# Performance work log

Measured on AMD Instinct MI355X. Metric: run time of the kernel, lower is better.

The kernel has to match this reference:

```python
import jax, jax.numpy as jnp
import numpy as np

N = 100000          # nodes
E = 1600000         # edges
KS = 3              # kernel_size per dim
DIM = 3             # pseudo-coordinate dim
CH = [1, 8, 16, 32, 16, 8, 1]
_BITS = ((0,0,0),(1,0,0),(0,1,0),(1,1,0),(0,0,1),(1,0,1),(0,1,1),(1,1,1))
_STRIDES = (1, KS, KS * KS)


def setup_inputs() -> dict:
    key = jax.random.key(0)
    ks = jax.random.split(key, 32)
    inp = {
        "x": jax.random.normal(ks[0], (N, 1), jnp.float32),
        "edge_index": jax.random.randint(ks[1], (2, E), 0, N),
        "pseudo": jax.random.uniform(ks[2], (E, DIM), dtype=jnp.float32),
    }
    ki = 3
    for i in range(6):
        fi, fo = CH[i], CH[i + 1]
        inp[f"w{i+1}"] = jax.random.normal(ks[ki], (KS**DIM, fi, fo), jnp.float32) / np.float32(np.sqrt(fi * 8)); ki += 1
        inp[f"root{i+1}"] = jax.random.normal(ks[ki], (fi, fo), jnp.float32) / np.float32(np.sqrt(fi)); ki += 1
        inp[f"b{i+1}"] = jnp.zeros((fo,), jnp.float32); ki += 1
    return inp


def spline_conv(x, src, dst, pseudo, W, root, bias):
    """Degree-1 open B-spline SplineConv, sum aggregation (norm=False) + root + bias.
    x: [N,Fin], pseudo: [E,DIM] in [0,1], W: [27,Fin,Fout]."""
    v = pseudo * (KS - 1)                              # [E,DIM] in [0,KS-1]
    f = jnp.clip(jnp.floor(v), 0.0, KS - 2)           # left knot per dim
    frac = v - f                                       # fractional part
    fi = f.astype(jnp.int32)
    # transform every node by all 27 kernel matrices once: [N,27,Fout]
    xw = jnp.einsum('nf,kfo->nko', x, W)
    m = jnp.zeros((src.shape[0], W.shape[-1]), x.dtype)
    for bits in _BITS:                                 # 2^DIM = 8 nonzero basis fns
        w = jnp.ones((src.shape[0],), x.dtype)
        idx = jnp.zeros((src.shape[0],), jnp.int32)
        for d in range(DIM):
            w = w * (frac[:, d] if bits[d] else (1.0 - frac[:, d]))
            idx = idx + (fi[:, d] + bits[d]) * _STRIDES[d]
        m = m + w[:, None] * xw[src, idx]              # gather [E,Fout]
    out = jax.ops.segment_sum(m, dst, num_segments=x.shape[0])
    return out + x @ root + bias


def reference(x, edge_index, pseudo, w1, root1, b1, w2, root2, b2, w3, root3, b3,
              w4, root4, b4, w5, root5, b5, w6, root6, b6):
    src, dst = edge_index[0], edge_index[1]
    h = x
    for (W, R, B) in ((w1, root1, b1), (w2, root2, b2), (w3, root3, b3),
                      (w4, root4, b4), (w5, root5, b5), (w6, root6, b6)):
        h = jax.nn.elu(spline_conv(h, src, dst, pseudo, W, R, B))
    return h.reshape(-1)
```

## Files before the change

kernel.cpp:

```cpp
#include <hip/hip_runtime.h>
#include <hip/hip_fp16.h>

#define N_NODES 100000
#define N_EDGES 1600000
#define TS      1024
#define NTILE   ((N_NODES + TS - 1) / TS)
#define NGRP    (NTILE * 8)
#define E_PAD2  (N_EDGES + NGRP * 64 + 256)
#define GRID_E2 (E_PAD2 / 256)

typedef _Float16 f16x8 __attribute__((ext_vector_type(8)));
typedef float    f32x4 __attribute__((ext_vector_type(4)));


__device__ __forceinline__ void pseudo_to_of(float p0, float p1, float p2,
                                             int& oct, float& fr0, float& fr1, float& fr2) {
    float v0 = p0 * 2.0f, v1 = p1 * 2.0f, v2 = p2 * 2.0f;
    int i0 = v0 >= 1.0f, i1 = v1 >= 1.0f, i2 = v2 >= 1.0f;
    fr0 = v0 - (float)i0; fr1 = v1 - (float)i1; fr2 = v2 - (float)i2;
    oct = i0 + 2 * i1 + 4 * i2;
}

template<int Fin>
__device__ __forceinline__ void loadanyT(const float* __restrict__ hp, float* x) {
    if constexpr (Fin % 4 == 0) {
        const float4* xv = reinterpret_cast<const float4*>(hp);
        #pragma unroll
        for (int f = 0; f < Fin / 4; ++f) {
            float4 t = xv[f];
            x[4*f+0] = t.x; x[4*f+1] = t.y; x[4*f+2] = t.z; x[4*f+3] = t.w;
        }
    } else {
        #pragma unroll
        for (int f = 0; f < Fin; ++f) x[f] = hp[f];
    }
}

template<int Fin>
__device__ __forceinline__ void loadanyT(const __half* __restrict__ hp, float* x) {
    if constexpr (Fin % 8 == 0) {
        #pragma unroll
        for (int r = 0; r < Fin / 8; ++r) {
            union { uint4 v; __half2 h2[4]; } u;
            u.v = ((const uint4*)hp)[r];
            #pragma unroll
            for (int q = 0; q < 4; ++q) {
                float2 f = __half22float2(u.h2[q]);
                x[r*8 + 2*q]     = f.x;
                x[r*8 + 2*q + 1] = f.y;
            }
        }
    } else {
        #pragma unroll
        for (int f = 0; f < Fin; ++f) x[f] = __half2float(hp[f]);
    }
}

template<int CH>
__device__ __forceinline__ void storeanyT(float* __restrict__ p, const float* z) {
    if constexpr (CH % 4 == 0) {
        #pragma unroll
        for (int o = 0; o < CH / 4; ++o) {
            float4 t; t.x = z[4*o]; t.y = z[4*o+1]; t.z = z[4*o+2]; t.w = z[4*o+3];
            ((float4*)p)[o] = t;
        }
    } else if constexpr (CH % 2 == 0) {
        #pragma unroll
        for (int o = 0; o < CH / 2; ++o) {
            float2 t; t.x = z[2*o]; t.y = z[2*o+1];
            ((float2*)p)[o] = t;
        }
    } else {
        #pragma unroll
        for (int o = 0; o < CH; ++o) p[o] = z[o];
    }
}

template<int CH>
__device__ __forceinline__ void storeanyT(__half* __restrict__ p, const float* z) {
    if constexpr (CH % 8 == 0) {
        #pragma unroll
        for (int q = 0; q < CH / 8; ++q) {
            union { uint4 v; __half2 h2[4]; } u;
            #pragma unroll
            for (int r = 0; r < 4; ++r)
                u.h2[r] = __floats2half2_rn(z[q*8 + 2*r], z[q*8 + 2*r + 1]);
            ((uint4*)p)[q] = u.v;
        }
    } else if constexpr (CH % 4 == 0) {
        #pragma unroll
        for (int q = 0; q < CH / 4; ++q) {
            union { uint2 v; __half2 h2[2]; } u;
            u.h2[0] = __floats2half2_rn(z[4*q],     z[4*q + 1]);
            u.h2[1] = __floats2half2_rn(z[4*q + 2], z[4*q + 3]);
            ((uint2*)p)[q] = u.v;
        }
    } else if constexpr (CH % 2 == 0) {
        #pragma unroll
        for (int q = 0; q < CH / 2; ++q)
            ((__half2*)p)[q] = __floats2half2_rn(z[2*q], z[2*q+1]);
    } else {
        #pragma unroll
        for (int o = 0; o < CH; ++o) p[o] = __float2half(z[o]);
    }
}

template<int CH>
__device__ __forceinline__ void accum_m_f16(float* acc, const __half* __restrict__ p) {
    if constexpr (CH % 8 == 0) {
        #pragma unroll
        for (int q = 0; q < CH / 8; ++q) {
            union { uint4 v; __half2 h2[4]; } u;
            u.v = ((const uint4*)p)[q];
            #pragma unroll
            for (int r = 0; r < 4; ++r) {
                float2 f = __half22float2(u.h2[r]);
                acc[q*8 + 2*r]     += f.x;
                acc[q*8 + 2*r + 1] += f.y;
            }
        }
    } else if constexpr (CH % 2 == 0) {
        #pragma unroll
        for (int q = 0; q < CH / 2; ++q) {
            float2 f = __half22float2(((const __half2*)p)[q]);
            acc[2*q] += f.x; acc[2*q+1] += f.y;
        }
    } else {
        #pragma unroll
        for (int o = 0; o < CH; ++o) acc[o] += __half2float(p[o]);
    }
}

__device__ __forceinline__ int cnt_unpack(unsigned v, int half) {
    return (int)((v >> (half * 16)) & 0xFFFFu);
}


__global__ __launch_bounds__(256) void count8_k(const int* __restrict__ dst,
                                                const float* __restrict__ pseudo,
                                                unsigned* __restrict__ cnt4,
                                                unsigned short* __restrict__ rank16) {
    int e = blockIdx.x * 256 + threadIdx.x;
    if (e >= N_EDGES) return;
    int d = dst[e];
    size_t pb = (size_t)e * 3;
    int oct; float a, b, c;
    pseudo_to_of(pseudo[pb], pseudo[pb + 1], pseudo[pb + 2], oct, a, b, c);
    unsigned inc = 1u << ((oct & 1) * 16);
    unsigned r = atomicAdd(&cnt4[d * 4 + (oct >> 1)], inc);
    rank16[e] = (unsigned short)cnt_unpack(r, oct & 1);
}

__global__ __launch_bounds__(256) void scan_g1(const unsigned* __restrict__ cnt4,
                                               int* __restrict__ gsum) {
    __shared__ int red[256];
    int g = blockIdx.x, t = threadIdx.x;
    int tile = g >> 3, oct = g & 7;
    int s = 0;
    #pragma unroll
    for (int q = 0; q < 4; ++q) {
        int n = tile * TS + t * 4 + q;
        if (n < N_NODES) s += cnt_unpack(cnt4[n * 4 + (oct >> 1)], oct & 1);
    }
    red[t] = s;
    __syncthreads();
    #pragma unroll
    for (int off = 128; off > 0; off >>= 1) {
        if (t < off) red[t] += red[t + off];
        __syncthreads();
    }
    if (t == 0) gsum[g] = red[0];
}

__global__ __launch_bounds__(1024) void scan_g2(const int* __restrict__ gsum,
                                                int* __restrict__ gbase,
                                                int* __restrict__ tot,
                                                unsigned char* __restrict__ winoct,
                                                uint4* __restrict__ slotmeta) {
    __shared__ int s[1024];
    __shared__ int sraw;
    int t = threadIdx.x;
    int v = 0;
    if (t < NGRP) v = ((gsum[t] + 63) >> 6) << 6;
    s[t] = v;
    __syncthreads();
    #pragma unroll
    for (int off = 1; off < 1024; off <<= 1) {
        int u = (t >= off) ? s[t - off] : 0;
        __syncthreads();
        s[t] += u;
        __syncthreads();
    }
    if (t < NGRP) gbase[t] = s[t] - v;
    if (t == NGRP - 1) sraw = s[t];
    __syncthreads();
    int raw = sraw;
    int totp = (raw + 255) & ~255;
    if (t == 0) { tot[0] = raw; tot[1] = totp; }
    int fill = totp - raw;
    if (t < fill) {
        uint4 z; z.x = z.y = z.z = z.w = 0u;
        slotmeta[raw + t] = z;
    }
    if (t < (fill >> 6)) winoct[(raw >> 6) + t] = 0;
}

__global__ __launch_bounds__(256) void scan_g3(const unsigned* __restrict__ cnt4,
                                               const int* __restrict__ gbase,
                                               int* __restrict__ slotstart,
                                               unsigned char* __restrict__ winoct,
                                               uint4* __restrict__ slotmeta) {
    __shared__ int s[256];
    int g = blockIdx.x, t = threadIdx.x;
    int tile = g >> 3, oct = g & 7;
    int c[4];
    int sum = 0;
    #pragma unroll
    for (int q = 0; q < 4; ++q) {
        int n = tile * TS + t * 4 + q;
        c[q] = (n < N_NODES) ? cnt_unpack(cnt4[n * 4 + (oct >> 1)], oct & 1) : 0;
        sum += c[q];
    }
    s[t] = sum;
    __syncthreads();
    #pragma unroll
    for (int off = 1; off < 256; off <<= 1) {
        int u = (t >= off) ? s[t - off] : 0;
        __syncthreads();
        s[t] += u;
        __syncthreads();
    }
    int base = gbase[g];
    int run = base + s[t] - sum;
    #pragma unroll
    for (int q = 0; q < 4; ++q) {
        int n = tile * TS + t * 4 + q;
        if (n < N_NODES) { slotstart[n * 8 + oct] = run; run += c[q]; }
    }
    int cntg = s[255];
    int padded = ((cntg + 63) >> 6) << 6;
    for (int w = t; w < (padded >> 6); w += 256)
        winoct[(base >> 6) + w] = (unsigned char)oct;
    for (int i = t; i < padded - cntg; i += 256) {
        uint4 z; z.x = z.y = z.z = z.w = 0u;
        slotmeta[base + cntg + i] = z;
    }
}

__global__ __launch_bounds__(256) void scatter2_k(const int* __restrict__ src,
                                                  const int* __restrict__ dst,
                                                  const float* __restrict__ pseudo,
                                                  const unsigned short* __restrict__ rank16,
                                                  const int* __restrict__ slotstart,
                                                  uint4* __restrict__ slotmeta) {
    int e = blockIdx.x * 256 + threadIdx.x;
    if (e >= N_EDGES) return;
    int d = dst[e];
    size_t pb = (size_t)e * 3;
    int oct; float fr0, fr1, fr2;
    pseudo_to_of(pseudo[pb], pseudo[pb + 1], pseudo[pb + 2], oct, fr0, fr1, fr2);
    int slot = slotstart[d * 8 + oct] + (int)rank16[e];
    union { uint4 v; struct { int s; __half2 f01; __half2 f2x; unsigned pad; } t; } su;
    su.t.s   = src[e];
    su.t.f01 = __floats2half2_rn(fr0, fr1);
    su.t.f2x = __floats2half2_rn(fr2, 0.0f);
    su.t.pad = 0u;
    slotmeta[slot] = su.v;
}


template<int Fin, int Fout>
__device__ __forceinline__ void wprep_elem(const float* __restrict__ W,
                                           _Float16* __restrict__ WB, int i) {
    constexpr int KT = (8 * Fin) / 32;
    constexpr int NT = (Fout + 15) / 16;
    int j    = i & 7;
    int lane = (i >> 3) & 63;
    int rest = i >> 9;
    int nt = rest % NT; rest /= NT;
    int kt = rest % KT;
    int g  = rest / KT;
    int kb = lane >> 4, n = lane & 15;
    int k  = kt * 32 + kb * 8 + j;
    int b  = k / Fin, f = k % Fin;
    int bidx = (g & 1) + 3 * ((g >> 1) & 1) + 9 * ((g >> 2) & 1);
    int idx  = bidx + (b & 1) + 3 * ((b >> 1) & 1) + 9 * ((b >> 2) & 1);
    int col  = nt * 16 + n;
    float v = (col < Fout) ? W[((size_t)idx * Fin + f) * Fout + col] : 0.0f;
    WB[i] = (_Float16)v;
}

#define WS2 8192
#define WS3 32768
#define WS4 32768
#define WS5 16384

__global__ __launch_bounds__(256) void wprep_all_k(const float* __restrict__ W2,
                                                   const float* __restrict__ W3,
                                                   const float* __restrict__ W4,
                                                   const float* __restrict__ W5,
                                                   _Float16* __restrict__ WB2,
                                                   _Float16* __restrict__ WB3,
                                                   _Float16* __restrict__ WB4,
                                                   _Float16* __restrict__ WB5) {
    int i = blockIdx.x * 256 + threadIdx.x;
    if (i < WS2) { wprep_elem<8, 16>(W2, WB2, i); return; }
    i -= WS2;
    if (i < WS3) { wprep_elem<16, 32>(W3, WB3, i); return; }
    i -= WS3;
    if (i < WS4) { wprep_elem<32, 16>(W4, WB4, i); return; }
    i -= WS4;
    if (i < WS5) { wprep_elem<16, 8>(W5, WB5, i); return; }
}


template<int Fin, int Fout>
__global__ __launch_bounds__(256) void msg_mfma_k(const __half* __restrict__ h,
                                                  const uint4* __restrict__ slotmeta,
                                                  const unsigned char* __restrict__ winoct,
                                                  const int* __restrict__ tot,
                                                  const _Float16* __restrict__ WB,
                                                  __half* __restrict__ m) {
    constexpr int KT = (8 * Fin) / 32;
    constexpr int NT = (Fout + 15) / 16;
    constexpr int LOG2FIN = (Fin == 8) ? 3 : (Fin == 16) ? 4 : 5;
    constexpr int ZR = NT * 16 + 8;

    __shared__ __align__(16) _Float16 zbuf[4][64 * ZR];

    const int base = blockIdx.x * 256;
    if (base >= tot[1]) return;

    const int tid = threadIdx.x, wv = tid >> 6, lane = tid & 63;
    const int slot = base + tid;
    const int wbase = base + wv * 64;
    const int kb = lane >> 4;

    int oct = winoct[(base >> 6) + wv];
    oct = __builtin_amdgcn_readfirstlane(oct);

    int   sE[4];
    float g0[4], h0[4], g1[4], h1[4], g2[4], h2v[4];
    #pragma unroll
    for (int mt = 0; mt < 4; ++mt) {
        union { uint4 v; struct { int s; __half2 f01; __half2 f2x; unsigned pad; } t; } u;
        u.v = slotmeta[wbase + mt * 16 + (lane & 15)];
        sE[mt] = u.t.s;
        float2 f01 = __half22float2(u.t.f01);
        float2 f2x = __half22float2(u.t.f2x);
        g0[mt] = 1.0f - f01.x; h0[mt] = f01.x;
        g1[mt] = 1.0f - f01.y; h1[mt] = f01.y;
        g2[mt] = 1.0f - f2x.x; h2v[mt] = f2x.x;
    }

    f32x4 acc[4][NT];
    #pragma unroll
    for (int mt = 0; mt < 4; ++mt)
        #pragma unroll
        for (int nt = 0; nt < NT; ++nt)
            acc[mt][nt] = (f32x4){0.0f, 0.0f, 0.0f, 0.0f};

    const f16x8* __restrict__ WBv = (const f16x8*)WB;
    const f16x8* __restrict__ hv  = (const f16x8*)h;

    #pragma unroll
    for (int kt = 0; kt < KT; ++kt) {
        f16x8 bf[NT];
        #pragma unroll
        for (int nt = 0; nt < NT; ++nt)
            bf[nt] = WBv[((oct * KT + kt) * NT + nt) * 64 + lane];

        const int k0 = kt * 32 + kb * 8;
        const int b  = k0 >> LOG2FIN;
        const int f8 = (k0 & (Fin - 1)) >> 3;

        #pragma unroll
        for (int mt = 0; mt < 4; ++mt) {
            f16x8 xa = hv[(size_t)sE[mt] * (Fin / 8) + f8];
            float w = ((b & 1) ? h0[mt] : g0[mt])
                    * ((b & 2) ? h1[mt] : g1[mt])
                    * ((b & 4) ? h2v[mt] : g2[mt]);
            _Float16 wh = (_Float16)w;
            f16x8 av;
            #pragma unroll
            for (int j = 0; j < 8; ++j) av[j] = xa[j] * wh;
            #pragma unroll
            for (int nt = 0; nt < NT; ++nt)
                acc[mt][nt] = __builtin_amdgcn_mfma_f32_16x16x32_f16(av, bf[nt], acc[mt][nt], 0, 0, 0);
        }
    }

    #pragma unroll
    for (int mt = 0; mt < 4; ++mt) {
        #pragma unroll
        for (int nt = 0; nt < NT; ++nt) {
            #pragma unroll
            for (int q = 0; q < 4; ++q) {
                int e = mt * 16 + (lane >> 4) * 4 + q;
                int o = nt * 16 + (lane & 15);
                zbuf[wv][e * ZR + o] = (_Float16)acc[mt][nt][q];
            }
        }
    }
    __syncthreads();

    constexpr int NV = (Fout * 2) / 16;
    const uint4* zr = (const uint4*)&zbuf[wv][lane * ZR];
    uint4* mp = (uint4*)(m + (size_t)slot * Fout);
    #pragma unroll
    for (int r = 0; r < NV; ++r) mp[r] = zr[r];
}


template<int Fin, int Fout, int CH, typename TIn>
__global__ __launch_bounds__(256) void msg_k(const TIn* __restrict__ h,
                                             const uint4* __restrict__ slotmeta,
                                             const unsigned char* __restrict__ winoct,
                                             const int* __restrict__ tot,
                                             const float* __restrict__ W,
                                             __half* __restrict__ m,
                                             int coff) {
    int base = blockIdx.x * 256;
    if (base >= tot[1]) return;
    int wv = threadIdx.x >> 6;
    int g = winoct[(base >> 6) + wv];
    g = __builtin_amdgcn_readfirstlane(g);
    const int bidx = (g & 1) + 3 * ((g >> 1) & 1) + 9 * ((g >> 2) & 1);

    int j = base + threadIdx.x;

    union { uint4 v; struct { int s; __half2 f01; __half2 f2x; unsigned pad; } t; } u;
    u.v = slotmeta[j];
    int s = u.t.s;
    float2 f01 = __half22float2(u.t.f01);
    float2 f2x = __half22float2(u.t.f2x);
    float fr0 = f01.x, fr1 = f01.y, fr2 = f2x.x;
    float a0[2] = {1.0f - fr0, fr0};
    float a1[2] = {1.0f - fr1, fr1};
    float a2[2] = {1.0f - fr2, fr2};
    float w[8];
    #pragma unroll
    for (int b = 0; b < 8; ++b)
        w[b] = a0[b & 1] * a1[(b >> 1) & 1] * a2[(b >> 2) & 1];

    float x[Fin];
    loadanyT<Fin>(h + (size_t)s * Fin, x);

    float z[CH];
    #pragma unroll
    for (int o = 0; o < CH; ++o) z[o] = 0.0f;

    #pragma unroll
    for (int b = 0; b < 8; ++b) {
        const int idx = bidx + (b & 1) + 3 * ((b >> 1) & 1) + 9 * ((b >> 2) & 1);
        const float* __restrict__ wp = W + (size_t)idx * (Fin * Fout) + coff;
        float wb = w[b];
        #pragma unroll
        for (int f = 0; f < Fin; ++f) {
            float a = wb * x[f];
            #pragma unroll
            for (int o = 0; o < CH; ++o) z[o] = fmaf(a, wp[f * Fout + o], z[o]);
        }
    }

    storeanyT<CH>(m + (size_t)j * CH, z);
}


template<int Fin, int Fout, int CH, typename TIn, typename TOut>
__global__ __launch_bounds__(256) void gather_k(const TIn* __restrict__ hin,
                                                const __half* __restrict__ m,
                                                const int* __restrict__ slotstart,
                                                const unsigned* __restrict__ cnt4,
                                                const float* __restrict__ root,
                                                const float* __restrict__ bias,
                                                TOut* __restrict__ hout,
                                                int coff) {
    int n = blockIdx.x * 256 + threadIdx.x;
    if (n >= N_NODES) return;

    float acc[CH];
    #pragma unroll
    for (int o = 0; o < CH; ++o) acc[o] = bias[coff + o];

    float x[Fin];
    loadanyT<Fin>(hin + (size_t)n * Fin, x);
    #pragma unroll
    for (int f = 0; f < Fin; ++f) {
        #pragma unroll
        for (int o = 0; o < CH; ++o)
            acc[o] = fmaf(x[f], root[f * Fout + coff + o], acc[o]);
    }

    int4 sa = ((const int4*)slotstart)[n * 2];
    int4 sb = ((const int4*)slotstart)[n * 2 + 1];
    uint4 cp = ((const uint4*)cnt4)[n];
    int ss[8] = {sa.x, sa.y, sa.z, sa.w, sb.x, sb.y, sb.z, sb.w};
    int cc[8];
    cc[0] = (int)(cp.x & 0xFFFFu); cc[1] = (int)(cp.x >> 16);
    cc[2] = (int)(cp.y & 0xFFFFu); cc[3] = (int)(cp.y >> 16);
    cc[4] = (int)(cp.z & 0xFFFFu); cc[5] = (int)(cp.z >> 16);
    cc[6] = (int)(cp.w & 0xFFFFu); cc[7] = (int)(cp.w >> 16);

    #pragma unroll
    for (int oct = 0; oct < 8; ++oct) {
        int p = ss[oct];
        for (int j = 0; j < cc[oct]; ++j)
            accum_m_f16<CH>(acc, m + (size_t)(p + j) * CH);
    }

    float zz[CH];
    #pragma unroll
    for (int o = 0; o < CH; ++o) {
        float t = acc[o];
        zz[o] = t > 0.0f ? t : expm1f(t);
    }
    storeanyT<CH>(hout + (size_t)n * Fout + coff, zz);
}


template<int Fin, int Fout>
__global__ __launch_bounds__(256) void init_out_k(const float* __restrict__ h,
                                                  const float* __restrict__ root,
                                                  const float* __restrict__ bias,
                                                  float* __restrict__ out) {
    int n = blockIdx.x * 256 + threadIdx.x;
    if (n >= N_NODES) return;
    float xr[Fin];
    #pragma unroll
    for (int f = 0; f < Fin; ++f) xr[f] = h[(size_t)n * Fin + f];
    float z[Fout];
    #pragma unroll
    for (int o = 0; o < Fout; ++o) z[o] = bias[o];
    #pragma unroll
    for (int f = 0; f < Fin; ++f)
        #pragma unroll
        for (int o = 0; o < Fout; ++o) z[o] += xr[f] * root[f * Fout + o];
    #pragma unroll
    for (int o = 0; o < Fout; ++o) out[(size_t)n * Fout + o] = z[o];
}

template<int Fin, int Fout>
__global__ __launch_bounds__(256) void edge_k(const float* __restrict__ h,
                                              const int* __restrict__ src,
                                              const int* __restrict__ dst,
                                              const float* __restrict__ pseudo,
                                              const float* __restrict__ W,
                                              float* __restrict__ out) {
    constexpr int KFF = Fin * Fout;
    constexpr int STRIDE = KFF + 1;
    __shared__ float sW[27 * STRIDE];
    for (int i = threadIdx.x; i < 27 * KFF; i += 256) {
        int k = i / KFF;
        sW[k * STRIDE + (i - k * KFF)] = W[i];
    }
    __syncthreads();
    int e = blockIdx.x * 256 + threadIdx.x;
    if (e >= N_EDGES) return;
    int s = src[e], d = dst[e];
    size_t pb = (size_t)e * 3;
    int oct; float fr0, fr1, fr2;
    pseudo_to_of(pseudo[pb], pseudo[pb+1], pseudo[pb+2], oct, fr0, fr1, fr2);
    int i0 = oct & 1, i1 = (oct >> 1) & 1, i2 = (oct >> 2) & 1;
    float a0[2] = {1.0f - fr0, fr0};
    float a1[2] = {1.0f - fr1, fr1};
    float a2[2] = {1.0f - fr2, fr2};
    float xr[Fin];
    #pragma unroll
    for (int f = 0; f < Fin; ++f) xr[f] = h[(size_t)s * Fin + f];
    float z[Fout];
    #pragma unroll
    for (int o = 0; o < Fout; ++o) z[o] = 0.0f;
    #pragma unroll
    for (int b = 0; b < 8; ++b) {
        int idx = (i0 + (b & 1)) + 3 * (i1 + ((b >> 1) & 1)) + 9 * (i2 + ((b >> 2) & 1));
        float wb = a0[b & 1] * a1[(b >> 1) & 1] * a2[(b >> 2) & 1];
        const float* wp = &sW[idx * STRIDE];
        #pragma unroll
        for (int f = 0; f < Fin; ++f) {
            float a = wb * xr[f];
            #pragma unroll
            for (int o = 0; o < Fout; ++o) z[o] += a * wp[f * Fout + o];
        }
    }
    float* op = out + (size_t)d * Fout;
    #pragma unroll
    for (int o = 0; o < Fout; ++o) atomicAdd(&op[o], z[o]);
}

__global__ __launch_bounds__(256) void elu_k(float* __restrict__ p, int total) {
    int i = blockIdx.x * 256 + threadIdx.x;
    if (i < total) {
        float t = p[i];
        p[i] = t > 0.0f ? t : expm1f(t);
    }
}


template<int Fin, int Fout, typename TIn, typename TOut>
static void run_layer_mfma(const TIn* hin, TOut* hout,
                           const float* root, const float* bias,
                           const uint4* slotmeta, const unsigned char* winoct,
                           const int* tot, const int* slotstart, const unsigned* cnt4,
                           const _Float16* WB, __half* m, hipStream_t stream) {
    msg_mfma_k<Fin, Fout><<<GRID_E2, 256, 0, stream>>>(hin, slotmeta, winoct, tot, WB, m);
    gather_k<Fin, Fout, Fout, TIn, TOut><<<(N_NODES + 255) / 256, 256, 0, stream>>>(
        hin, m, slotstart, cnt4, root, bias, hout, 0);
}

template<int Fin, int Fout, typename TIn, typename TOut>
static void run_layer_valu(const TIn* hin, TOut* hout,
                           const float* W, const float* root, const float* bias,
                           const uint4* slotmeta, const unsigned char* winoct,
                           const int* tot, const int* slotstart, const unsigned* cnt4,
                           __half* m, int chunk, hipStream_t stream) {
    const int GN = (N_NODES + 255) / 256;
    if (Fout <= chunk) {
        msg_k<Fin, Fout, Fout, TIn><<<GRID_E2, 256, 0, stream>>>(hin, slotmeta, winoct, tot, W, m, 0);
        gather_k<Fin, Fout, Fout, TIn, TOut><<<GN, 256, 0, stream>>>(hin, m, slotstart, cnt4, root, bias, hout, 0);
        return;
    }
    if constexpr (Fout > 16) {
        if (chunk == 16) {
            for (int p = 0; p < Fout / 16; ++p) {
                msg_k<Fin, Fout, 16, TIn><<<GRID_E2, 256, 0, stream>>>(hin, slotmeta, winoct, tot, W, m, 16 * p);
                gather_k<Fin, Fout, 16, TIn, TOut><<<GN, 256, 0, stream>>>(hin, m, slotstart, cnt4, root, bias, hout, 16 * p);
            }
            return;
        }
    }
    if constexpr (Fout > 8) {
        if (chunk == 8) {
            for (int p = 0; p < Fout / 8; ++p) {
                msg_k<Fin, Fout, 8, TIn><<<GRID_E2, 256, 0, stream>>>(hin, slotmeta, winoct, tot, W, m, 8 * p);
                gather_k<Fin, Fout, 8, TIn, TOut><<<GN, 256, 0, stream>>>(hin, m, slotstart, cnt4, root, bias, hout, 8 * p);
            }
            return;
        }
    }
    if constexpr (Fout > 4) {
        if (chunk == 4) {
            for (int p = 0; p < Fout / 4; ++p) {
                msg_k<Fin, Fout, 4, TIn><<<GRID_E2, 256, 0, stream>>>(hin, slotmeta, winoct, tot, W, m, 4 * p);
                gather_k<Fin, Fout, 4, TIn, TOut><<<GN, 256, 0, stream>>>(hin, m, slotstart, cnt4, root, bias, hout, 4 * p);
            }
            return;
        }
    }
    if constexpr (Fout > 2) {
        if (chunk == 2) {
            for (int p = 0; p < Fout / 2; ++p) {
                msg_k<Fin, Fout, 2, TIn><<<GRID_E2, 256, 0, stream>>>(hin, slotmeta, winoct, tot, W, m, 2 * p);
                gather_k<Fin, Fout, 2, TIn, TOut><<<GN, 256, 0, stream>>>(hin, m, slotstart, cnt4, root, bias, hout, 2 * p);
            }
            return;
        }
    }
}

template<int Fin, int Fout>
static void run_layer_old(const float* hin, float* hout,
                          const float* W, const float* root, const float* bias,
                          const int* src, const int* dst, const float* pseudo,
                          hipStream_t stream) {
    init_out_k<Fin, Fout><<<(N_NODES + 255) / 256, 256, 0, stream>>>(hin, root, bias, hout);
    edge_k<Fin, Fout><<<(N_EDGES + 255) / 256, 256, 0, stream>>>(hin, src, dst, pseudo, W, hout);
    int total = N_NODES * Fout;
    elu_k<<<(total + 255) / 256, 256, 0, stream>>>(hout, total);
}

extern "C" void kernel_launch(void* const* d_in, const int* in_sizes, int n_in,
                              void* d_out, int out_size, void* d_ws, size_t ws_size,
                              hipStream_t stream) {
    const float* x      = (const float*)d_in[0];
    const int*   ei     = (const int*)d_in[1];
    const float* pseudo = (const float*)d_in[2];
    const int* src = ei;
    const int* dst = ei + N_EDGES;

    const float* W[6]; const float* R[6]; const float* B[6];
    for (int i = 0; i < 6; ++i) {
        W[i] = (const float*)d_in[3 + 3 * i];
        R[i] = (const float*)d_in[4 + 3 * i];
        B[i] = (const float*)d_in[5 + 3 * i];
    }
    float* out = (float*)d_out;
    char* ws = (char*)d_ws;

    const int tiers[5] = {32, 16, 8, 4, 2};
    int chunk = 0;
    size_t o_hA = 0, o_hB = 0, o_c4 = 0, o_ss = 0, o_rk = 0, o_meta = 0,
           o_wo = 0, o_sm = 0, o_wb = 0, o_m = 0;
    for (int t = 0; t < 5; ++t) {
        int c = tiers[t];
        size_t off = 0;
        auto alloc = [&](size_t bytes) { size_t cur = off; off = (off + bytes + 255) & ~(size_t)255; return cur; };
        size_t a_hA   = alloc((size_t)N_NODES * 32 * 2);
        size_t a_hB   = alloc((size_t)N_NODES * 32 * 2);
        size_t a_c4   = alloc((size_t)N_NODES * 4 * 4);
        size_t a_ss   = alloc((size_t)N_NODES * 8 * 4);
        size_t a_rk   = alloc((size_t)N_EDGES * 2);
        size_t a_meta = alloc((size_t)(2 * NGRP + 8) * 4);
        size_t a_wo   = alloc((size_t)(E_PAD2 / 64));
        size_t a_sm   = alloc((size_t)E_PAD2 * 16);
        size_t a_wb   = alloc((size_t)4 * 65536 * 2);
        size_t a_m    = alloc((size_t)E_PAD2 * c * 2);
        if (off <= ws_size) {
            chunk = c;
            o_hA = a_hA; o_hB = a_hB; o_c4 = a_c4; o_ss = a_ss; o_rk = a_rk;
            o_meta = a_meta; o_wo = a_wo; o_sm = a_sm; o_wb = a_wb; o_m = a_m;
            break;
        }
    }

    if (chunk > 0) {
        __half* hA     = (__half*)(ws + o_hA);
        __half* hB     = (__half*)(ws + o_hB);
        unsigned* cnt4 = (unsigned*)(ws + o_c4);
        int*   slotst  = (int*)(ws + o_ss);
        unsigned short* rank16 = (unsigned short*)(ws + o_rk);
        int*   gsum    = (int*)(ws + o_meta);
        int*   gbase   = gsum + NGRP;
        int*   tot     = gbase + NGRP;
        unsigned char* winoct = (unsigned char*)(ws + o_wo);
        uint4* slotmeta= (uint4*)(ws + o_sm);
        _Float16* WB2  = (_Float16*)(ws + o_wb);
        _Float16* WB3  = WB2 + 65536;
        _Float16* WB4  = WB2 + 2 * 65536;
        _Float16* WB5  = WB2 + 3 * 65536;
        __half* m      = (__half*)(ws + o_m);

        hipMemsetAsync(cnt4, 0, (size_t)N_NODES * 4 * 4, stream);

        count8_k<<<N_EDGES / 256, 256, 0, stream>>>(dst, pseudo, cnt4, rank16);
        scan_g1<<<NGRP, 256, 0, stream>>>(cnt4, gsum);
        scan_g2<<<1, 1024, 0, stream>>>(gsum, gbase, tot, winoct, slotmeta);
        scan_g3<<<NGRP, 256, 0, stream>>>(cnt4, gbase, slotst, winoct, slotmeta);
        scatter2_k<<<N_EDGES / 256, 256, 0, stream>>>(src, dst, pseudo, rank16, slotst, slotmeta);

        if (chunk == 32) {
            wprep_all_k<<<(WS2 + WS3 + WS4 + WS5 + 255) / 256, 256, 0, stream>>>(
                W[1], W[2], W[3], W[4], WB2, WB3, WB4, WB5);

            run_layer_valu<1, 8, float, __half>(x, hA, W[0], R[0], B[0], slotmeta, winoct, tot,
                                                slotst, cnt4, m, chunk, stream);
            run_layer_mfma<8, 16, __half, __half>(hA, hB, R[1], B[1], slotmeta, winoct, tot,
                                                  slotst, cnt4, WB2, m, stream);
            run_layer_mfma<16, 32, __half, __half>(hB, hA, R[2], B[2], slotmeta, winoct, tot,
                                                   slotst, cnt4, WB3, m, stream);
            run_layer_mfma<32, 16, __half, __half>(hA, hB, R[3], B[3], slotmeta, winoct, tot,
                                                   slotst, cnt4, WB4, m, stream);
            run_layer_mfma<16, 8, __half, __half>(hB, hA, R[4], B[4], slotmeta, winoct, tot,
                                                  slotst, cnt4, WB5, m, stream);
            run_layer_valu<8, 1, __half, float>(hA, out, W[5], R[5], B[5], slotmeta, winoct, tot,
                                                slotst, cnt4, m, chunk, stream);
        } else {
            run_layer_valu<1, 8, float, __half>(x, hA, W[0], R[0], B[0], slotmeta, winoct, tot,
                                                slotst, cnt4, m, chunk, stream);
            run_layer_valu<8, 16, __half, __half>(hA, hB, W[1], R[1], B[1], slotmeta, winoct, tot,
                                                  slotst, cnt4, m, chunk, stream);
            run_layer_valu<16, 32, __half, __half>(hB, hA, W[2], R[2], B[2], slotmeta, winoct, tot,
                                                   slotst, cnt4, m, chunk, stream);
            run_layer_valu<32, 16, __half, __half>(hA, hB, W[3], R[3], B[3], slotmeta, winoct, tot,
                                                   slotst, cnt4, m, chunk, stream);
            run_layer_valu<16, 8, __half, __half>(hB, hA, W[4], R[4], B[4], slotmeta, winoct, tot,
                                                  slotst, cnt4, m, chunk, stream);
            run_layer_valu<8, 1, __half, float>(hA, out, W[5], R[5], B[5], slotmeta, winoct, tot,
                                                slotst, cnt4, m, chunk, stream);
        }
    } else {
        float* hAf = (float*)ws;
        float* hBf = hAf + (size_t)N_NODES * 32;
        run_layer_old<1, 8>  (x,   hAf, W[0], R[0], B[0], src, dst, pseudo, stream);
        run_layer_old<8, 16> (hAf, hBf, W[1], R[1], B[1], src, dst, pseudo, stream);
        run_layer_old<16, 32>(hBf, hAf, W[2], R[2], B[2], src, dst, pseudo, stream);
        run_layer_old<32, 16>(hAf, hBf, W[3], R[3], B[3], src, dst, pseudo, stream);
        run_layer_old<16, 8> (hBf, hAf, W[4], R[4], B[4], src, dst, pseudo, stream);
        run_layer_old<8, 1>  (hAf, out, W[5], R[5], B[5], src, dst, pseudo, stream);
    }
}
```

Measured before the change: 398.7 us.

## Split per-node gather across four threads with shuffle reduction

The gather kernel now assigns four threads per destination node. Each thread handles two of the eight octant message segments and a quarter of the root input features. Partial accumulators are combined with xor shuffles, and each thread applies ELU and stores a slice of the output channels. This adds parallelism and memory-level concurrency to the latency-bound, degree-imbalanced gather. The cost is redundant shuffle work and four times as many threads.

```diff
diff --git a/kernel.cpp b/kernel.cpp
--- a/kernel.cpp
+++ b/kernel.cpp
@@ -54,6 +54,38 @@
         #pragma unroll
         for (int f = 0; f < Fin; ++f) x[f] = __half2float(hp[f]);
     }
+}
+
+template<int Q>
+__device__ __forceinline__ void loadq(const __half* __restrict__ hp, float* x) {
+    if constexpr (Q == 2) {
+        union { unsigned v; __half2 h2; } u;
+        u.v = *(const unsigned*)hp;
+        float2 f = __half22float2(u.h2);
+        x[0] = f.x; x[1] = f.y;
+    } else if constexpr (Q == 4) {
+        union { uint2 v; __half2 h2[2]; } u;
+        u.v = *(const uint2*)hp;
+        float2 a = __half22float2(u.h2[0]);
+        float2 b = __half22float2(u.h2[1]);
+        x[0] = a.x; x[1] = a.y; x[2] = b.x; x[3] = b.y;
+    } else if constexpr (Q == 8) {
+        union { uint4 v; __half2 h2[4]; } u;
+        u.v = *(const uint4*)hp;
+        #pragma unroll
+        for (int q = 0; q < 4; ++q) {
+            float2 f = __half22float2(u.h2[q]);
+            x[2*q] = f.x; x[2*q+1] = f.y;
+        }
+    } else {
+        #pragma unroll
+        for (int f = 0; f < Q; ++f) x[f] = __half2float(hp[f]);
+    }
+}
+template<int Q>
+__device__ __forceinline__ void loadq(const float* __restrict__ hp, float* x) {
+    #pragma unroll
+    for (int f = 0; f < Q; ++f) x[f] = hp[f];
 }
 
 template<int CH>
@@ -468,54 +500,85 @@
 
 
 template<int Fin, int Fout, int CH, typename TIn, typename TOut>
-__global__ __launch_bounds__(256) void gather_k(const TIn* __restrict__ hin,
-                                                const __half* __restrict__ m,
-                                                const int* __restrict__ slotstart,
-                                                const unsigned* __restrict__ cnt4,
-                                                const float* __restrict__ root,
-                                                const float* __restrict__ bias,
-                                                TOut* __restrict__ hout,
-                                                int coff) {
-    int n = blockIdx.x * 256 + threadIdx.x;
+__global__ __launch_bounds__(256) void gather4_k(const TIn* __restrict__ hin,
+                                                 const __half* __restrict__ m,
+                                                 const int* __restrict__ slotstart,
+                                                 const unsigned* __restrict__ cnt4,
+                                                 const float* __restrict__ root,
+                                                 const float* __restrict__ bias,
+                                                 TOut* __restrict__ hout,
+                                                 int coff) {
+    int gid = blockIdx.x * 256 + threadIdx.x;
+    int n = gid >> 2, sub = gid & 3;
     if (n >= N_NODES) return;
 
     float acc[CH];
     #pragma unroll
-    for (int o = 0; o < CH; ++o) acc[o] = bias[coff + o];
-
-    float x[Fin];
-    loadanyT<Fin>(hin + (size_t)n * Fin, x);
-    #pragma unroll
-    for (int f = 0; f < Fin; ++f) {
-        #pragma unroll
-        for (int o = 0; o < CH; ++o)
-            acc[o] = fmaf(x[f], root[f * Fout + coff + o], acc[o]);
-    }
-
-    int4 sa = ((const int4*)slotstart)[n * 2];
-    int4 sb = ((const int4*)slotstart)[n * 2 + 1];
-    uint4 cp = ((const uint4*)cnt4)[n];
-    int ss[8] = {sa.x, sa.y, sa.z, sa.w, sb.x, sb.y, sb.z, sb.w};
-    int cc[8];
-    cc[0] = (int)(cp.x & 0xFFFFu); cc[1] = (int)(cp.x >> 16);
-    cc[2] = (int)(cp.y & 0xFFFFu); cc[3] = (int)(cp.y >> 16);
-    cc[4] = (int)(cp.z & 0xFFFFu); cc[5] = (int)(cp.z >> 16);
-    cc[6] = (int)(cp.w & 0xFFFFu); cc[7] = (int)(cp.w >> 16);
-
-    #pragma unroll
-    for (int oct = 0; oct < 8; ++oct) {
-        int p = ss[oct];
-        for (int j = 0; j < cc[oct]; ++j)
-            accum_m_f16<CH>(acc, m + (size_t)(p + j) * CH);
-    }
-
-    float zz[CH];
+    for (int o = 0; o < CH; ++o) acc[o] = 0.0f;
+
+    if constexpr (Fin >= 4 && (Fin % 4) == 0) {
+        constexpr int Q = Fin / 4;
+        float x[Q];
+        loadq<Q>(hin + (size_t)n * Fin + sub * Q, x);
+        #pragma unroll
+        for (int f = 0; f < Q; ++f) {
+            #pragma unroll
+            for (int o = 0; o < CH; ++o)
+                acc[o] = fmaf(x[f], root[(sub * Q + f) * Fout + coff + o], acc[o]);
+        }
+    } else {
+        if (sub == 0) {
+            float x[Fin];
+            loadanyT<Fin>(hin + (size_t)n * Fin, x);
+            #pragma unroll
+            for (int f = 0; f < Fin; ++f) {
+                #pragma unroll
+                for (int o = 0; o < CH; ++o)
+                    acc[o] = fmaf(x[f], root[f * Fout + coff + o], acc[o]);
+            }
+        }
+    }
+    if (sub == 0) {
+        #pragma unroll
+        for (int o = 0; o < CH; ++o) acc[o] += bias[coff + o];
+    }
+
+    int2 sp = ((const int2*)slotstart)[n * 4 + sub];
+    unsigned cp = cnt4[n * 4 + sub];
+    int c0 = (int)(cp & 0xFFFFu), c1 = (int)(cp >> 16);
+    for (int j = 0; j < c0; ++j)
+        accum_m_f16<CH>(acc, m + (size_t)(sp.x + j) * CH);
+    for (int j = 0; j < c1; ++j)
+        accum_m_f16<CH>(acc, m + (size_t)(sp.y + j) * CH);
+
     #pragma unroll
     for (int o = 0; o < CH; ++o) {
-        float t = acc[o];
-        zz[o] = t > 0.0f ? t : expm1f(t);
-    }
-    storeanyT<CH>(hout + (size_t)n * Fout + coff, zz);
+        acc[o] += __shfl_xor(acc[o], 1);
+        acc[o] += __shfl_xor(acc[o], 2);
+    }
+
+    if constexpr ((CH % 4) == 0) {
+        constexpr int PER = CH / 4;
+        float zz[PER];
+        #pragma unroll
+        for (int i = 0; i < PER; ++i) {
+            float t = acc[sub * PER + i];
+            zz[i] = t > 0.0f ? t : expm1f(t);
+        }
+        storeanyT<PER>(hout + (size_t)n * Fout + coff + sub * PER, zz);
+    } else {
+        const int per = (CH + 3) / 4;
+        int c0i = sub * per;
+        #pragma unroll 4
+        for (int i = 0; i < per; ++i) {
+            int o = c0i + i;
+            if (o < CH) {
+                float t = acc[o];
+                t = t > 0.0f ? t : expm1f(t);
+                hout[(size_t)n * Fout + coff + o] = (TOut)t;
+            }
+        }
+    }
 }
 
 
@@ -597,6 +660,8 @@
 }
 
 
+#define GN4 ((N_NODES * 4 + 255) / 256)
+
 template<int Fin, int Fout, typename TIn, typename TOut>
 static void run_layer_mfma(const TIn* hin, TOut* hout,
                            const float* root, const float* bias,
@@ -604,7 +669,7 @@
                            const int* tot, const int* slotstart, const unsigned* cnt4,
                            const _Float16* WB, __half* m, hipStream_t stream) {
     msg_mfma_k<Fin, Fout><<<GRID_E2, 256, 0, stream>>>(hin, slotmeta, winoct, tot, WB, m);
-    gather_k<Fin, Fout, Fout, TIn, TOut><<<(N_NODES + 255) / 256, 256, 0, stream>>>(
+    gather4_k<Fin, Fout, Fout, TIn, TOut><<<GN4, 256, 0, stream>>>(
         hin, m, slotstart, cnt4, root, bias, hout, 0);
 }
 
@@ -614,17 +679,16 @@
                            const uint4* slotmeta, const unsigned char* winoct,
                            const int* tot, const int* slotstart, const unsigned* cnt4,
                            __half* m, int chunk, hipStream_t stream) {
-    const int GN = (N_NODES + 255) / 256;
     if (Fout <= chunk) {
         msg_k<Fin, Fout, Fout, TIn><<<GRID_E2, 256, 0, stream>>>(hin, slotmeta, winoct, tot, W, m, 0);
-        gather_k<Fin, Fout, Fout, TIn, TOut><<<GN, 256, 0, stream>>>(hin, m, slotstart, cnt4, root, bias, hout, 0);
+        gather4_k<Fin, Fout, Fout, TIn, TOut><<<GN4, 256, 0, stream>>>(hin, m, slotstart, cnt4, root, bias, hout, 0);
         return;
     }
     if constexpr (Fout > 16) {
         if (chunk == 16) {
             for (int p = 0; p < Fout / 16; ++p) {
                 msg_k<Fin, Fout, 16, TIn><<<GRID_E2, 256, 0, stream>>>(hin, slotmeta, winoct, tot, W, m, 16 * p);
-                gather_k<Fin, Fout, 16, TIn, TOut><<<GN, 256, 0, stream>>>(hin, m, slotstart, cnt4, root, bias, hout, 16 * p);
+                gather4_k<Fin, Fout, 16, TIn, TOut><<<GN4, 256, 0, stream>>>(hin, m, slotstart, cnt4, root, bias, hout, 16 * p);
             }
             return;
         }
@@ -633,7 +697,7 @@
         if (chunk == 8) {
             for (int p = 0; p < Fout / 8; ++p) {
                 msg_k<Fin, Fout, 8, TIn><<<GRID_E2, 256, 0, stream>>>(hin, slotmeta, winoct, tot, W, m, 8 * p);
-                gather_k<Fin, Fout, 8, TIn, TOut><<<GN, 256, 0, stream>>>(hin, m, slotstart, cnt4, root, bias, hout, 8 * p);
+                gather4_k<Fin, Fout, 8, TIn, TOut><<<GN4, 256, 0, stream>>>(hin, m, slotstart, cnt4, root, bias, hout, 8 * p);
             }
             return;
         }
@@ -642,7 +706,7 @@
         if (chunk == 4) {
             for (int p = 0; p < Fout / 4; ++p) {
                 msg_k<Fin, Fout, 4, TIn><<<GRID_E2, 256, 0, stream>>>(hin, slotmeta, winoct, tot, W, m, 4 * p);
-                gather_k<Fin, Fout, 4, TIn, TOut><<<GN, 256, 0, stream>>>(hin, m, slotstart, cnt4, root, bias, hout, 4 * p);
+                gather4_k<Fin, Fout, 4, TIn, TOut><<<GN4, 256, 0, stream>>>(hin, m, slotstart, cnt4, root, bias, hout, 4 * p);
             }
             return;
         }
@@ -651,7 +715,7 @@
         if (chunk == 2) {
             for (int p = 0; p < Fout / 2; ++p) {
                 msg_k<Fin, Fout, 2, TIn><<<GRID_E2, 256, 0, stream>>>(hin, slotmeta, winoct, tot, W, m, 2 * p);
-                gather_k<Fin, Fout, 2, TIn, TOut><<<GN, 256, 0, stream>>>(hin, m, slotstart, cnt4, root, bias, hout, 2 * p);
+                gather4_k<Fin, Fout, 2, TIn, TOut><<<GN4, 256, 0, stream>>>(hin, m, slotstart, cnt4, root, bias, hout, 2 * p);
             }
             return;
         }
```

New measurement: 412.1 us. +3.4%, slower.

## Fuse MFMA message and node aggregation into per-tile kernels with LDS atomics

Applied to the files above, without the earlier changes.

Replaces the two-kernel MFMA layers, which wrote per-edge fp16 messages to global memory and then gathered them per node, with one kernel per 128-node tile. That kernel accumulates MFMA results into a shared-memory float buffer using LDS atomics, then applies root, bias and ELU in place. The aim is to remove the large per-edge message write and read and the extra launch for each middle layer. To support this, the node tile shrinks to 128, the scan kernels are reshaped, a local destination row is packed into the slot metadata, and the workspace tiers drop the 32-wide chunk. Risks are LDS atomic contention, lower occupancy from the big shared buffer, and the first and last VALU layers now running with a smaller chunk.

```diff
diff --git a/kernel.cpp b/kernel.cpp
--- a/kernel.cpp
+++ b/kernel.cpp
@@ -3,7 +3,7 @@
 
 #define N_NODES 100000
 #define N_EDGES 1600000
-#define TS      1024
+#define TS      128
 #define NTILE   ((N_NODES + TS - 1) / TS)
 #define NGRP    (NTILE * 8)
 #define E_PAD2  (N_EDGES + NGRP * 64 + 256)
@@ -151,21 +151,16 @@
     rank16[e] = (unsigned short)cnt_unpack(r, oct & 1);
 }
 
-__global__ __launch_bounds__(256) void scan_g1(const unsigned* __restrict__ cnt4,
+__global__ __launch_bounds__(128) void scan_g1(const unsigned* __restrict__ cnt4,
                                                int* __restrict__ gsum) {
-    __shared__ int red[256];
+    __shared__ int red[128];
     int g = blockIdx.x, t = threadIdx.x;
     int tile = g >> 3, oct = g & 7;
-    int s = 0;
-    #pragma unroll
-    for (int q = 0; q < 4; ++q) {
-        int n = tile * TS + t * 4 + q;
-        if (n < N_NODES) s += cnt_unpack(cnt4[n * 4 + (oct >> 1)], oct & 1);
-    }
-    red[t] = s;
+    int n = tile * TS + t;
+    red[t] = (n < N_NODES) ? cnt_unpack(cnt4[n * 4 + (oct >> 1)], oct & 1) : 0;
     __syncthreads();
     #pragma unroll
-    for (int off = 128; off > 0; off >>= 1) {
+    for (int off = 64; off > 0; off >>= 1) {
         if (t < off) red[t] += red[t + off];
         __syncthreads();
     }
@@ -177,72 +172,73 @@
                                                 int* __restrict__ tot,
                                                 unsigned char* __restrict__ winoct,
                                                 uint4* __restrict__ slotmeta) {
-    __shared__ int s[1024];
+    const int CHN = (NGRP + 1023) / 1024;
+    __shared__ int ssum[1024];
     __shared__ int sraw;
     int t = threadIdx.x;
-    int v = 0;
-    if (t < NGRP) v = ((gsum[t] + 63) >> 6) << 6;
-    s[t] = v;
+    int pv[CHN];
+    int s = 0;
+    #pragma unroll
+    for (int j = 0; j < CHN; ++j) {
+        int i = t * CHN + j;
+        pv[j] = (i < NGRP) ? (((gsum[i] + 63) >> 6) << 6) : 0;
+        s += pv[j];
+    }
+    ssum[t] = s;
     __syncthreads();
     #pragma unroll
     for (int off = 1; off < 1024; off <<= 1) {
+        int u = (t >= off) ? ssum[t - off] : 0;
+        __syncthreads();
+        ssum[t] += u;
+        __syncthreads();
+    }
+    int run = (t == 0) ? 0 : ssum[t - 1];
+    #pragma unroll
+    for (int j = 0; j < CHN; ++j) {
+        int i = t * CHN + j;
+        if (i < NGRP) { gbase[i] = run; run += pv[j]; }
+    }
+    if (t == 1023) sraw = ssum[1023];
+    __syncthreads();
+    int raw = sraw;
+    int totp = (raw + 255) & ~255;
+    if (t == 0) { gbase[NGRP] = raw; tot[0] = raw; tot[1] = totp; }
+    int fill = totp - raw;
+    if (t < fill) {
+        uint4 z; z.x = z.y = z.z = 0u; z.w = (unsigned)TS;
+        slotmeta[raw + t] = z;
+    }
+    if (t < (fill >> 6)) winoct[(raw >> 6) + t] = 0;
+}
+
+__global__ __launch_bounds__(128) void scan_g3(const unsigned* __restrict__ cnt4,
+                                               const int* __restrict__ gbase,
+                                               int* __restrict__ slotstart,
+                                               unsigned char* __restrict__ winoct,
+                                               uint4* __restrict__ slotmeta) {
+    __shared__ int s[128];
+    int g = blockIdx.x, t = threadIdx.x;
+    int tile = g >> 3, oct = g & 7;
+    int n = tile * TS + t;
+    int c = (n < N_NODES) ? cnt_unpack(cnt4[n * 4 + (oct >> 1)], oct & 1) : 0;
+    s[t] = c;
+    __syncthreads();
+    #pragma unroll
+    for (int off = 1; off < 128; off <<= 1) {
         int u = (t >= off) ? s[t - off] : 0;
         __syncthreads();
         s[t] += u;
         __syncthreads();
     }
-    if (t < NGRP) gbase[t] = s[t] - v;
-    if (t == NGRP - 1) sraw = s[t];
-    __syncthreads();
-    int raw = sraw;
-    int totp = (raw + 255) & ~255;
-    if (t == 0) { tot[0] = raw; tot[1] = totp; }
-    int fill = totp - raw;
-    if (t < fill) {
-        uint4 z; z.x = z.y = z.z = z.w = 0u;
-        slotmeta[raw + t] = z;
-    }
-    if (t < (fill >> 6)) winoct[(raw >> 6) + t] = 0;
-}
-
-__global__ __launch_bounds__(256) void scan_g3(const unsigned* __restrict__ cnt4,
-                                               const int* __restrict__ gbase,
-                                               int* __restrict__ slotstart,
-                                               unsigned char* __restrict__ winoct,
-                                               uint4* __restrict__ slotmeta) {
-    __shared__ int s[256];
-    int g = blockIdx.x, t = threadIdx.x;
-    int tile = g >> 3, oct = g & 7;
-    int c[4];
-    int sum = 0;
-    #pragma unroll
-    for (int q = 0; q < 4; ++q) {
-        int n = tile * TS + t * 4 + q;
-        c[q] = (n < N_NODES) ? cnt_unpack(cnt4[n * 4 + (oct >> 1)], oct & 1) : 0;
-        sum += c[q];
-    }
-    s[t] = sum;
-    __syncthreads();
-    #pragma unroll
-    for (int off = 1; off < 256; off <<= 1) {
-        int u = (t >= off) ? s[t - off] : 0;
-        __syncthreads();
-        s[t] += u;
-        __syncthreads();
-    }
     int base = gbase[g];
-    int run = base + s[t] - sum;
-    #pragma unroll
-    for (int q = 0; q < 4; ++q) {
-        int n = tile * TS + t * 4 + q;
-        if (n < N_NODES) { slotstart[n * 8 + oct] = run; run += c[q]; }
-    }
-    int cntg = s[255];
+    if (n < N_NODES) slotstart[n * 8 + oct] = base + s[t] - c;
+    int cntg = s[127];
     int padded = ((cntg + 63) >> 6) << 6;
-    for (int w = t; w < (padded >> 6); w += 256)
+    for (int w = t; w < (padded >> 6); w += 128)
         winoct[(base >> 6) + w] = (unsigned char)oct;
-    for (int i = t; i < padded - cntg; i += 256) {
-        uint4 z; z.x = z.y = z.z = z.w = 0u;
+    for (int i = t; i < padded - cntg; i += 128) {
+        uint4 z; z.x = z.y = z.z = 0u; z.w = (unsigned)TS;
         slotmeta[base + cntg + i] = z;
     }
 }
@@ -264,7 +260,7 @@
     su.t.s   = src[e];
     su.t.f01 = __floats2half2_rn(fr0, fr1);
     su.t.f2x = __floats2half2_rn(fr2, 0.0f);
-    su.t.pad = 0u;
+    su.t.pad = (unsigned)(d & (TS - 1));
     slotmeta[slot] = su.v;
 }
 
@@ -315,100 +311,128 @@
 
 
 template<int Fin, int Fout>
-__global__ __launch_bounds__(256) void msg_mfma_k(const __half* __restrict__ h,
-                                                  const uint4* __restrict__ slotmeta,
-                                                  const unsigned char* __restrict__ winoct,
-                                                  const int* __restrict__ tot,
-                                                  const _Float16* __restrict__ WB,
-                                                  __half* __restrict__ m) {
+__global__ __launch_bounds__(256) void fused_mfma_k(const __half* __restrict__ h,
+                                                    const uint4* __restrict__ slotmeta,
+                                                    const unsigned char* __restrict__ winoct,
+                                                    const int* __restrict__ gbase,
+                                                    const _Float16* __restrict__ WB,
+                                                    const float* __restrict__ root,
+                                                    const float* __restrict__ bias,
+                                                    __half* __restrict__ hout) {
     constexpr int KT = (8 * Fin) / 32;
     constexpr int NT = (Fout + 15) / 16;
     constexpr int LOG2FIN = (Fin == 8) ? 3 : (Fin == 16) ? 4 : 5;
-    constexpr int ZR = NT * 16 + 8;
-
-    __shared__ __align__(16) _Float16 zbuf[4][64 * ZR];
-
-    const int base = blockIdx.x * 256;
-    if (base >= tot[1]) return;
-
+    constexpr int AS = Fout + 1;
+    constexpr int REM = Fout & 15;
+
+    __shared__ float accs[(TS + 1) * AS];
+    __shared__ unsigned short sld[4][64];
+
+    const int tile = blockIdx.x;
     const int tid = threadIdx.x, wv = tid >> 6, lane = tid & 63;
-    const int slot = base + tid;
-    const int wbase = base + wv * 64;
+
+    for (int i = tid; i < (TS + 1) * AS; i += 256) accs[i] = 0.0f;
+    __syncthreads();
+
+    const int s0 = gbase[tile * 8];
+    const int s1 = gbase[tile * 8 + 8];
     const int kb = lane >> 4;
-
-    int oct = winoct[(base >> 6) + wv];
-    oct = __builtin_amdgcn_readfirstlane(oct);
-
-    int   sE[4];
-    float g0[4], h0[4], g1[4], h1[4], g2[4], h2v[4];
-    #pragma unroll
-    for (int mt = 0; mt < 4; ++mt) {
-        union { uint4 v; struct { int s; __half2 f01; __half2 f2x; unsigned pad; } t; } u;
-        u.v = slotmeta[wbase + mt * 16 + (lane & 15)];
-        sE[mt] = u.t.s;
-        float2 f01 = __half22float2(u.t.f01);
-        float2 f2x = __half22float2(u.t.f2x);
-        g0[mt] = 1.0f - f01.x; h0[mt] = f01.x;
-        g1[mt] = 1.0f - f01.y; h1[mt] = f01.y;
-        g2[mt] = 1.0f - f2x.x; h2v[mt] = f2x.x;
-    }
-
-    f32x4 acc[4][NT];
-    #pragma unroll
-    for (int mt = 0; mt < 4; ++mt)
-        #pragma unroll
-        for (int nt = 0; nt < NT; ++nt)
-            acc[mt][nt] = (f32x4){0.0f, 0.0f, 0.0f, 0.0f};
-
     const f16x8* __restrict__ WBv = (const f16x8*)WB;
     const f16x8* __restrict__ hv  = (const f16x8*)h;
 
-    #pragma unroll
-    for (int kt = 0; kt < KT; ++kt) {
-        f16x8 bf[NT];
-        #pragma unroll
-        for (int nt = 0; nt < NT; ++nt)
-            bf[nt] = WBv[((oct * KT + kt) * NT + nt) * 64 + lane];
-
-        const int k0 = kt * 32 + kb * 8;
-        const int b  = k0 >> LOG2FIN;
-        const int f8 = (k0 & (Fin - 1)) >> 3;
-
+    for (int wbase = s0 + wv * 64; wbase < s1; wbase += 256) {
+        int oct = winoct[wbase >> 6];
+        oct = __builtin_amdgcn_readfirstlane(oct);
+
+        int   sE[4];
+        float g0[4], h0[4], g1[4], h1[4], g2[4], h2v[4];
         #pragma unroll
         for (int mt = 0; mt < 4; ++mt) {
-            f16x8 xa = hv[(size_t)sE[mt] * (Fin / 8) + f8];
-            float w = ((b & 1) ? h0[mt] : g0[mt])
-                    * ((b & 2) ? h1[mt] : g1[mt])
-                    * ((b & 4) ? h2v[mt] : g2[mt]);
-            _Float16 wh = (_Float16)w;
-            f16x8 av;
-            #pragma unroll
-            for (int j = 0; j < 8; ++j) av[j] = xa[j] * wh;
+            union { uint4 v; struct { int s; __half2 f01; __half2 f2x; unsigned pad; } t; } u;
+            u.v = slotmeta[wbase + mt * 16 + (lane & 15)];
+            sE[mt] = u.t.s;
+            if (lane < 16) sld[wv][mt * 16 + lane] = (unsigned short)u.t.pad;
+            float2 f01 = __half22float2(u.t.f01);
+            float2 f2x = __half22float2(u.t.f2x);
+            g0[mt] = 1.0f - f01.x; h0[mt] = f01.x;
+            g1[mt] = 1.0f - f01.y; h1[mt] = f01.y;
+            g2[mt] = 1.0f - f2x.x; h2v[mt] = f2x.x;
+        }
+
+        f32x4 accr[4][NT];
+        #pragma unroll
+        for (int mt = 0; mt < 4; ++mt)
             #pragma unroll
             for (int nt = 0; nt < NT; ++nt)
-                acc[mt][nt] = __builtin_amdgcn_mfma_f32_16x16x32_f16(av, bf[nt], acc[mt][nt], 0, 0, 0);
-        }
-    }
-
-    #pragma unroll
-    for (int mt = 0; mt < 4; ++mt) {
-        #pragma unroll
-        for (int nt = 0; nt < NT; ++nt) {
+                accr[mt][nt] = (f32x4){0.0f, 0.0f, 0.0f, 0.0f};
+
+        #pragma unroll
+        for (int kt = 0; kt < KT; ++kt) {
+            f16x8 bf[NT];
+            #pragma unroll
+            for (int nt = 0; nt < NT; ++nt)
+                bf[nt] = WBv[((oct * KT + kt) * NT + nt) * 64 + lane];
+
+            const int k0 = kt * 32 + kb * 8;
+            const int b  = k0 >> LOG2FIN;
+            const int f8 = (k0 & (Fin - 1)) >> 3;
+
+            #pragma unroll
+            for (int mt = 0; mt < 4; ++mt) {
+                f16x8 xa = hv[(size_t)sE[mt] * (Fin / 8) + f8];
+                float w = ((b & 1) ? h0[mt] : g0[mt])
+                        * ((b & 2) ? h1[mt] : g1[mt])
+                        * ((b & 4) ? h2v[mt] : g2[mt]);
+                _Float16 wh = (_Float16)w;
+                f16x8 av;
+                #pragma unroll
+                for (int j = 0; j < 8; ++j) av[j] = xa[j] * wh;
+                #pragma unroll
+                for (int nt = 0; nt < NT; ++nt)
+                    accr[mt][nt] = __builtin_amdgcn_mfma_f32_16x16x32_f16(av, bf[nt], accr[mt][nt], 0, 0, 0);
+            }
+        }
+
+        #pragma unroll
+        for (int mt = 0; mt < 4; ++mt) {
             #pragma unroll
             for (int q = 0; q < 4; ++q) {
                 int e = mt * 16 + (lane >> 4) * 4 + q;
-                int o = nt * 16 + (lane & 15);
-                zbuf[wv][e * ZR + o] = (_Float16)acc[mt][nt][q];
+                int r = (int)sld[wv][e];
+                float* ap = &accs[r * AS + (lane & 15)];
+                #pragma unroll
+                for (int nt = 0; nt < NT; ++nt) {
+                    bool ok = (REM == 0) || (nt < NT - 1) || ((lane & 15) < REM);
+                    if (ok) atomicAdd(&ap[nt * 16], accr[mt][nt][q]);
+                }
             }
         }
     }
     __syncthreads();
 
-    constexpr int NV = (Fout * 2) / 16;
-    const uint4* zr = (const uint4*)&zbuf[wv][lane * ZR];
-    uint4* mp = (uint4*)(m + (size_t)slot * Fout);
-    #pragma unroll
-    for (int r = 0; r < NV; ++r) mp[r] = zr[r];
+    if (tid < TS) {
+        int n = tile * TS + tid;
+        if (n < N_NODES) {
+            float xr[Fin];
+            loadanyT<Fin>(h + (size_t)n * Fin, xr);
+            float z[Fout];
+            #pragma unroll
+            for (int o = 0; o < Fout; ++o) z[o] = bias[o] + accs[tid * AS + o];
+            #pragma unroll
+            for (int f = 0; f < Fin; ++f) {
+                #pragma unroll
+                for (int o = 0; o < Fout; ++o)
+                    z[o] = fmaf(xr[f], root[f * Fout + o], z[o]);
+            }
+            float zz[Fout];
+            #pragma unroll
+            for (int o = 0; o < Fout; ++o) {
+                float t = z[o];
+                zz[o] = t > 0.0f ? t : expm1f(t);
+            }
+            storeanyT<Fout>(hout + (size_t)n * Fout, zz);
+        }
+    }
 }
 
 
@@ -598,17 +622,6 @@
 
 
 template<int Fin, int Fout, typename TIn, typename TOut>
-static void run_layer_mfma(const TIn* hin, TOut* hout,
-                           const float* root, const float* bias,
-                           const uint4* slotmeta, const unsigned char* winoct,
-                           const int* tot, const int* slotstart, const unsigned* cnt4,
-                           const _Float16* WB, __half* m, hipStream_t stream) {
-    msg_mfma_k<Fin, Fout><<<GRID_E2, 256, 0, stream>>>(hin, slotmeta, winoct, tot, WB, m);
-    gather_k<Fin, Fout, Fout, TIn, TOut><<<(N_NODES + 255) / 256, 256, 0, stream>>>(
-        hin, m, slotstart, cnt4, root, bias, hout, 0);
-}
-
-template<int Fin, int Fout, typename TIn, typename TOut>
 static void run_layer_valu(const TIn* hin, TOut* hout,
                            const float* W, const float* root, const float* bias,
                            const uint4* slotmeta, const unsigned char* winoct,
@@ -687,11 +700,12 @@
     float* out = (float*)d_out;
     char* ws = (char*)d_ws;
 
-    const int tiers[5] = {32, 16, 8, 4, 2};
+    const int tiers[3] = {8, 4, 2};
     int chunk = 0;
+    int fused = 0;
     size_t o_hA = 0, o_hB = 0, o_c4 = 0, o_ss = 0, o_rk = 0, o_meta = 0,
            o_wo = 0, o_sm = 0, o_wb = 0, o_m = 0;
-    for (int t = 0; t < 5; ++t) {
+    for (int t = 0; t < 3; ++t) {
         int c = tiers[t];
         size_t off = 0;
         auto alloc = [&](size_t bytes) { size_t cur = off; off = (off + bytes + 255) & ~(size_t)255; return cur; };
@@ -700,13 +714,13 @@
         size_t a_c4   = alloc((size_t)N_NODES * 4 * 4);
         size_t a_ss   = alloc((size_t)N_NODES * 8 * 4);
         size_t a_rk   = alloc((size_t)N_EDGES * 2);
-        size_t a_meta = alloc((size_t)(2 * NGRP + 8) * 4);
+        size_t a_meta = alloc((size_t)(2 * NGRP + 16) * 4);
         size_t a_wo   = alloc((size_t)(E_PAD2 / 64));
         size_t a_sm   = alloc((size_t)E_PAD2 * 16);
         size_t a_wb   = alloc((size_t)4 * 65536 * 2);
         size_t a_m    = alloc((size_t)E_PAD2 * c * 2);
         if (off <= ws_size) {
-            chunk = c;
+            chunk = c; fused = (t == 0);
             o_hA = a_hA; o_hB = a_hB; o_c4 = a_c4; o_ss = a_ss; o_rk = a_rk;
             o_meta = a_meta; o_wo = a_wo; o_sm = a_sm; o_wb = a_wb; o_m = a_m;
             break;
@@ -721,7 +735,7 @@
         unsigned short* rank16 = (unsigned short*)(ws + o_rk);
         int*   gsum    = (int*)(ws + o_meta);
         int*   gbase   = gsum + NGRP;
-        int*   tot     = gbase + NGRP;
+        int*   tot     = gbase + NGRP + 1;
         unsigned char* winoct = (unsigned char*)(ws + o_wo);
         uint4* slotmeta= (uint4*)(ws + o_sm);
         _Float16* WB2  = (_Float16*)(ws + o_wb);
@@ -733,25 +747,21 @@
         hipMemsetAsync(cnt4, 0, (size_t)N_NODES * 4 * 4, stream);
 
         count8_k<<<N_EDGES / 256, 256, 0, stream>>>(dst, pseudo, cnt4, rank16);
-        scan_g1<<<NGRP, 256, 0, stream>>>(cnt4, gsum);
+        scan_g1<<<NGRP, 128, 0, stream>>>(cnt4, gsum);
         scan_g2<<<1, 1024, 0, stream>>>(gsum, gbase, tot, winoct, slotmeta);
-        scan_g3<<<NGRP, 256, 0, stream>>>(cnt4, gbase, slotst, winoct, slotmeta);
+        scan_g3<<<NGRP, 128, 0, stream>>>(cnt4, gbase, slotst, winoct, slotmeta);
         scatter2_k<<<N_EDGES / 256, 256, 0, stream>>>(src, dst, pseudo, rank16, slotst, slotmeta);
 
-        if (chunk == 32) {
+        if (fused) {
             wprep_all_k<<<(WS2 + WS3 + WS4 + WS5 + 255) / 256, 256, 0, stream>>>(
                 W[1], W[2], W[3], W[4], WB2, WB3, WB4, WB5);
 
             run_layer_valu<1, 8, float, __half>(x, hA, W[0], R[0], B[0], slotmeta, winoct, tot,
                                                 slotst, cnt4, m, chunk, stream);
-            run_layer_mfma<8, 16, __half, __half>(hA, hB, R[1], B[1], slotmeta, winoct, tot,
-                                                  slotst, cnt4, WB2, m, stream);
-            run_layer_mfma<16, 32, __half, __half>(hB, hA, R[2], B[2], slotmeta, winoct, tot,
-                                                   slotst, cnt4, WB3, m, stream);
-            run_layer_mfma<32, 16, __half, __half>(hA, hB, R[3], B[3], slotmeta, winoct, tot,
-                                                   slotst, cnt4, WB4, m, stream);
-            run_layer_mfma<16, 8, __half, __half>(hB, hA, R[4], B[4], slotmeta, winoct, tot,
-                                                  slotst, cnt4, WB5, m, stream);
+            fused_mfma_k<8, 16><<<NTILE, 256, 0, stream>>>(hA, slotmeta, winoct, gbase, WB2, R[1], B[1], hB);
+            fused_mfma_k<16, 32><<<NTILE, 256, 0, stream>>>(hB, slotmeta, winoct, gbase, WB3, R[2], B[2], hA);
+            fused_mfma_k<32, 16><<<NTILE, 256, 0, stream>>>(hA, slotmeta, winoct, gbase, WB4, R[3], B[3], hB);
+            fused_mfma_k<16, 8><<<NTILE, 256, 0, stream>>>(hB, slotmeta, winoct, gbase, WB5, R[4], B[4], hA);
             run_layer_valu<8, 1, __half, float>(hA, out, W[5], R[5], B[5], slotmeta, winoct, tot,
                                                 slotst, cnt4, m, chunk, stream);
         } else {
```

Result: slower. 1.119 ms (+180.7%).
